# Kernel tuning notes

Measured on AMD Instinct MI355X. Metric: run time of the kernel, lower is better.

Reference implementation:

```python
import jax, jax.numpy as jnp
import numpy as np

# Model dims derived from layers=[1024,2048,2048,2048,2048]
B = 4096
SUM_EVEN = 4096  # 0 + 2048 + 2048
SUM_ODD = 4096   # 2048 + 2048
D1 = 2048        # layers[1]: width of Ux
BLK = 2048


def rho(x):
    return jax.nn.sigmoid(4.0 * (x - 0.5))


def make_mask():
    # Staircase block pattern from layer_slices():
    # (rows 0:2048, cols 0:2048), (rows 0:2048, cols 2048:4096), (rows 2048:4096, cols 2048:4096)
    m = np.zeros((SUM_EVEN, SUM_ODD), dtype=np.float32)
    m[0:BLK, 0:BLK] = 1.0
    m[0:BLK, BLK:2 * BLK] = 1.0
    m[BLK:2 * BLK, BLK:2 * BLK] = 1.0
    return jnp.asarray(m)


def setup_inputs() -> dict:
    key = jax.random.key(0)
    k1, k2, k3 = jax.random.split(key, 3)
    xavier_std = 0.02  # ~ sqrt(2/(2048+2048)) per block
    W_mask = make_mask()
    W_tensor = jax.random.normal(k1, (SUM_EVEN, SUM_ODD), jnp.float32) * xavier_std
    W_tensor = W_tensor * W_mask  # enforce staircase sparsity at init
    return {
        "Ux": jax.random.normal(k2, (B, D1), jnp.float32),
        "s": jax.random.normal(k3, (B, SUM_EVEN), jnp.float32),
        "W_tensor": W_tensor,
        "b_even": jnp.zeros((1, SUM_EVEN), jnp.float32),
        "b_odd": jnp.zeros((1, SUM_ODD), jnp.float32),
        "W_mask": W_mask,
    }


def reference(Ux, s, W_tensor, b_even, b_odd, W_mask):
    # s_new = rho(rho(s) @ W + b_odd [+ Ux on first D1 cols]) @ W.T + b_even
    W = W_tensor * W_mask  # masked staircase matrix
    s_odd = rho(s) @ W + b_odd                 # [B, SUM_ODD]
    s_odd = s_odd.at[:, :D1].add(Ux)           # x only feeds first hidden layer
    return rho(s_odd) @ W.T + b_even           # [B, SUM_EVEN]
```

## Files before the change

### kernel.cpp

```cpp
#include <hip/hip_runtime.h>
#include <hip/hip_bf16.h>


#define N_DIM 4096
#define D1_DIM 2048

typedef short short8 __attribute__((ext_vector_type(8)));
typedef float f32x4 __attribute__((ext_vector_type(4)));

__device__ __forceinline__ float rho_f(float x) {
    return 1.0f / (1.0f + __expf(2.0f - 4.0f * x));
}

__device__ __forceinline__ unsigned short f2bf(float x) {
    unsigned int u = __builtin_bit_cast(unsigned int, x);
    u += 0x7fffu + ((u >> 16) & 1u);
    return (unsigned short)(u >> 16);
}

__device__ __forceinline__ void gl_lds16(const unsigned short* g, void* l) {
    __builtin_amdgcn_global_load_lds(
        (const __attribute__((address_space(1))) void*)g,
        (__attribute__((address_space(3))) void*)l, 16, 0, 0);
}

__global__ __launch_bounds__(256) void prep_kernel(
    const float* __restrict__ s, const float* __restrict__ W,
    unsigned short* __restrict__ Rs, unsigned short* __restrict__ Wb,
    unsigned short* __restrict__ WTb) {
    __shared__ unsigned short t[32][33];
    const int id = blockIdx.x;
    if (id < 16384) {
        const int bx = id & 127, by = id >> 7;
        if (by * 32 >= D1_DIM && bx * 32 < D1_DIM) return;
        const int tx = threadIdx.x & 31, ty = threadIdx.x >> 5;
        const int x = bx * 32 + tx;
        #pragma unroll
        for (int r = 0; r < 4; r++) {
            const int y = by * 32 + ty + r * 8;
            const size_t idx = (size_t)y * N_DIM + x;
            const unsigned short b = f2bf(W[idx]);
            Wb[idx] = b;
            t[ty + r * 8][tx] = b;
        }
        __syncthreads();
        #pragma unroll
        for (int r = 0; r < 4; r++) {
            const int yy = ty + r * 8;
            WTb[(size_t)(bx * 32 + yy) * N_DIM + (by * 32 + tx)] = t[tx][yy];
        }
    } else {
        const int n8 = (N_DIM * N_DIM) / 8;
        const int stride = 2048 * 256;
        for (int i = (id - 16384) * 256 + threadIdx.x; i < n8; i += stride) {
            float4 a = ((const float4*)s)[2 * i];
            float4 b = ((const float4*)s)[2 * i + 1];
            unsigned int r0 = f2bf(rho_f(a.x)) | ((unsigned int)f2bf(rho_f(a.y)) << 16);
            unsigned int r1 = f2bf(rho_f(a.z)) | ((unsigned int)f2bf(rho_f(a.w)) << 16);
            unsigned int r2 = f2bf(rho_f(b.x)) | ((unsigned int)f2bf(rho_f(b.y)) << 16);
            unsigned int r3 = f2bf(rho_f(b.z)) | ((unsigned int)f2bf(rho_f(b.w)) << 16);
            uint4 o; o.x = r0; o.y = r1; o.z = r2; o.w = r3;
            ((uint4*)Rs)[i] = o;
        }
    }
}

template<int MODE>
__global__ __launch_bounds__(1024, 4) void gemm_kernel(
    const unsigned short* __restrict__ A,
    const unsigned short* __restrict__ Bt,
    void* __restrict__ Out,
    const float* __restrict__ Ux,
    const float* __restrict__ bias) {
    __shared__ __align__(16) char lds[163840];

    const int id = blockIdx.x;
    const int wg = ((id & 7) << 5) | (id >> 3);
    const int by = wg >> 4, bx = wg & 15;
    const int brow = by << 8, bcol = bx << 8;

    const int tid = threadIdx.x;
    const int w = tid >> 6;
    const int L = tid & 63;
    const int wr = w >> 2;
    const int wc = w & 3;
    const int fr = L & 15;
    const int fq = L >> 4;
    const int swz = fr & 7;

    int kbeg, kend;
    if (MODE == 1) { kbeg = 0; kend = (bcol < D1_DIM) ? D1_DIM : N_DIM; }
    else           { kbeg = (bcol < D1_DIM) ? 0 : D1_DIM; kend = N_DIM; }

    const int srl = w * 8 + (L >> 3);
    const int schunk8 = ((L & 7) ^ (L >> 3)) << 3;
    const int wbase = w * 1024;
#define STAGEF(mat, gb, kcol, base) do {                                       \
        const unsigned short* g0_ = (mat) +                                    \
            (size_t)((gb) + srl) * N_DIM + (kcol) + schunk8;                   \
        gl_lds16(g0_, lds + (base) + wbase);                                   \
        gl_lds16(g0_ + 128 * N_DIM, lds + (base) + 16384 + wbase);             \
    } while (0)

    short8 af[2][4], bf[4];
#define LDA_K(ab, ks) do {                                                     \
        _Pragma("unroll") for (int m_ = 0; m_ < 4; ++m_) {                     \
            const int R_ = wr * 64 + m_ * 16 + fr;                             \
            af[ks][m_] = *(const short8*)(lds + (ab) + R_ * 128 +              \
                ((((ks) * 4 + fq) ^ swz) << 4)); }                             \
    } while (0)
#define LDB_K(bb, ks) do {                                                     \
        _Pragma("unroll") for (int n_ = 0; n_ < 4; ++n_) {                     \
            const int R_ = wc * 64 + n_ * 16 + fr;                             \
            bf[n_] = *(const short8*)(lds + (bb) + R_ * 128 +                  \
                ((((ks) * 4 + fq) ^ swz) << 4)); }                             \
    } while (0)

    f32x4 acc[4][4];
    #pragma unroll
    for (int i = 0; i < 4; i++)
        #pragma unroll
        for (int j = 0; j < 4; j++)
            acc[i][j] = (f32x4){0.f, 0.f, 0.f, 0.f};

#define MFMA_K(ks) do {                                                        \
        __builtin_amdgcn_s_setprio(1);                                         \
        _Pragma("unroll") for (int m_ = 0; m_ < 4; ++m_)                       \
        _Pragma("unroll") for (int n_ = 0; n_ < 4; ++n_)                       \
            acc[m_][n_] = __builtin_amdgcn_mfma_f32_16x16x32_bf16(             \
                af[ks][m_], bf[n_], acc[m_][n_], 0, 0, 0);                     \
        __builtin_amdgcn_s_setprio(0);                                         \
    } while (0)

#define SBAR0() __builtin_amdgcn_sched_barrier(0)
#define LGKM(n) do { asm volatile("s_waitcnt lgkmcnt(" #n ")" ::: "memory");   \
                     SBAR0(); } while (0)
#define BAR() __builtin_amdgcn_s_barrier()

    const int nk = (kend - kbeg) >> 6;
    const int km = nk - 1;

    {
        const int k0 = kbeg;
        const int k1 = kbeg + ((1 & km) << 6);
        STAGEF(A, brow, k0, 0);       STAGEF(Bt, bcol, k0, 98304);
        STAGEF(A, brow, k1, 32768);   STAGEF(Bt, bcol, k1, 131072);
        asm volatile("s_waitcnt vmcnt(4)" ::: "memory");
        BAR();
    }

    int ai = 0, si = 2;
    for (int t = 0; t < nk; ++t) {
        const int aB = ai * 32768;
        const int sA = si * 32768;
        const int bB = 98304 + (t & 1) * 32768;
        const int ka = kbeg + (((t + 2) & km) << 6);

        STAGEF(A, brow, ka, sA);
        LDA_K(aB, 0); SBAR0();
        LDB_K(bB, 0); SBAR0();
        LDA_K(aB, 1); SBAR0();
        LGKM(4);
        MFMA_K(0);
        LDB_K(bB, 1); SBAR0();
        LGKM(0);
        MFMA_K(1);
        BAR();
        STAGEF(Bt, bcol, ka, bB);
        asm volatile("s_waitcnt vmcnt(4)" ::: "memory");
        BAR();
        ai++; if (ai == 3) ai = 0;
        si++; if (si == 3) si = 0;
    }
    asm volatile("s_waitcnt vmcnt(0)" ::: "memory");

    const bool hasUx = (MODE == 1) && (bcol < D1_DIM);
    #pragma unroll
    for (int m = 0; m < 4; m++) {
        const int row0 = brow + wr * 64 + m * 16 + fq * 4;
        #pragma unroll
        for (int n = 0; n < 4; n++) {
            const int col = bcol + wc * 64 + n * 16 + fr;
            const float bv = bias[col];
            #pragma unroll
            for (int r = 0; r < 4; r++) {
                const int row = row0 + r;
                float v = acc[m][n][r] + bv;
                if (MODE == 1) {
                    if (hasUx) v += Ux[(size_t)row * D1_DIM + col];
                    ((unsigned short*)Out)[(size_t)row * N_DIM + col] =
                        f2bf(rho_f(v));
                } else {
                    ((float*)Out)[(size_t)row * N_DIM + col] = v;
                }
            }
        }
    }
#undef STAGEF
#undef LDA_K
#undef LDB_K
#undef MFMA_K
#undef SBAR0
#undef LGKM
#undef BAR
}

extern "C" void kernel_launch(void* const* d_in, const int* in_sizes, int n_in,
                              void* d_out, int out_size, void* d_ws, size_t ws_size,
                              hipStream_t stream) {
    const float* Ux     = (const float*)d_in[0];
    const float* s      = (const float*)d_in[1];
    const float* W      = (const float*)d_in[2];
    const float* b_even = (const float*)d_in[3];
    const float* b_odd  = (const float*)d_in[4];

    char* ws = (char*)d_ws;
    const size_t SZ = (size_t)N_DIM * N_DIM * 2;
    unsigned short* Rs  = (unsigned short*)(ws);
    unsigned short* R2  = (unsigned short*)(ws + SZ);
    unsigned short* Wb  = (unsigned short*)(ws + 2 * SZ);
    unsigned short* WTb = (unsigned short*)(ws + 3 * SZ);

    prep_kernel<<<18432, 256, 0, stream>>>(s, W, Rs, Wb, WTb);
    gemm_kernel<1><<<256, 1024, 0, stream>>>(Rs, WTb, (void*)R2, Ux, b_odd);
    gemm_kernel<2><<<256, 1024, 0, stream>>>(R2, Wb, d_out, Ux, b_even);
}
```

Before: 248.5 us.

## Shrink GEMM tiles to 256x128 with BK=32 and schedule heavy tiles first

Each GEMM block now covers a 256x128 output tile with 8 waves instead of 256x256 with 16 waves, and the K step drops from 64 to 32. The pipeline is simplified to one three-buffer ring holding A and B, with one barrier per step, using 72KB of LDS instead of 160KB. Blocks are ordered so that the tiles with the longer K range (4096 vs 2048, given the staircase mask) launch first. The aim is better load balance across CUs and more resident blocks, at the cost of less data reuse per tile, more loop iterations and barriers, and removal of the earlier split-fragment MFMA/LDS interleaving.

```diff
diff --git a/kernel.cpp b/kernel.cpp
--- a/kernel.cpp
+++ b/kernel.cpp
@@ -66,110 +66,97 @@
 }
 
 template<int MODE>
-__global__ __launch_bounds__(1024, 4) void gemm_kernel(
+__global__ __launch_bounds__(512, 4) void gemm_kernel(
     const unsigned short* __restrict__ A,
     const unsigned short* __restrict__ Bt,
     void* __restrict__ Out,
     const float* __restrict__ Ux,
     const float* __restrict__ bias) {
-    __shared__ __align__(16) char lds[163840];
+    __shared__ __align__(16) char lds[73728];
 
     const int id = blockIdx.x;
-    const int wg = ((id & 7) << 5) | (id >> 3);
-    const int by = wg >> 4, bx = wg & 15;
-    const int brow = by << 8, bcol = bx << 8;
+    const int grp = id >> 8;
+    const int i = id & 255;
+    const int tile = ((i & 7) << 5) | (i >> 3);
+    const int by = tile >> 4;
+    const int bxg = tile & 15;
+    int bx;
+    if (MODE == 1) bx = grp ? bxg : 16 + bxg;
+    else           bx = grp ? 16 + bxg : bxg;
+    const int brow = by << 8;
+    const int bcol = bx << 7;
 
     const int tid = threadIdx.x;
     const int w = tid >> 6;
     const int L = tid & 63;
-    const int wr = w >> 2;
-    const int wc = w & 3;
+    const int wr = w >> 1;
+    const int wc = w & 1;
     const int fr = L & 15;
     const int fq = L >> 4;
-    const int swz = fr & 7;
 
     int kbeg, kend;
     if (MODE == 1) { kbeg = 0; kend = (bcol < D1_DIM) ? D1_DIM : N_DIM; }
     else           { kbeg = (bcol < D1_DIM) ? 0 : D1_DIM; kend = N_DIM; }
 
-    const int srl = w * 8 + (L >> 3);
-    const int schunk8 = ((L & 7) ^ (L >> 3)) << 3;
-    const int wbase = w * 1024;
-#define STAGEF(mat, gb, kcol, base) do {                                       \
-        const unsigned short* g0_ = (mat) +                                    \
-            (size_t)((gb) + srl) * N_DIM + (kcol) + schunk8;                   \
-        gl_lds16(g0_, lds + (base) + wbase);                                   \
-        gl_lds16(g0_ + 128 * N_DIM, lds + (base) + 16384 + wbase);             \
+    const int srow = tid >> 2;
+    const int schunk = (tid & 3) ^ ((srow >> 1) & 3);
+    const unsigned short* gA0 = A + (size_t)(brow + srow) * N_DIM + schunk * 8;
+    const unsigned short* gA1 = gA0 + 128 * N_DIM;
+    const unsigned short* gB0 = Bt + (size_t)(bcol + srow) * N_DIM + schunk * 8;
+    const int dst16 = tid * 16;
+#define STAGE(kcol, bi) do {                                                   \
+        gl_lds16(gA0 + (kcol), lds + (bi) * 16384 + dst16);                    \
+        gl_lds16(gA1 + (kcol), lds + (bi) * 16384 + 8192 + dst16);             \
+        gl_lds16(gB0 + (kcol), lds + 49152 + (bi) * 8192 + dst16);             \
     } while (0)
 
-    short8 af[2][4], bf[4];
-#define LDA_K(ab, ks) do {                                                     \
-        _Pragma("unroll") for (int m_ = 0; m_ < 4; ++m_) {                     \
-            const int R_ = wr * 64 + m_ * 16 + fr;                             \
-            af[ks][m_] = *(const short8*)(lds + (ab) + R_ * 128 +              \
-                ((((ks) * 4 + fq) ^ swz) << 4)); }                             \
-    } while (0)
-#define LDB_K(bb, ks) do {                                                     \
-        _Pragma("unroll") for (int n_ = 0; n_ < 4; ++n_) {                     \
-            const int R_ = wc * 64 + n_ * 16 + fr;                             \
-            bf[n_] = *(const short8*)(lds + (bb) + R_ * 128 +                  \
-                ((((ks) * 4 + fq) ^ swz) << 4)); }                             \
+    const int slotb = (fq ^ ((fr >> 1) & 3)) << 4;
+    short8 af[4], bf[4];
+#define LDFRAGS(bi) do {                                                       \
+        const char* ab_ = lds + (bi) * 16384;                                  \
+        const char* bb_ = lds + 49152 + (bi) * 8192;                           \
+        _Pragma("unroll") for (int m_ = 0; m_ < 4; ++m_)                       \
+            af[m_] = *(const short8*)(ab_ + (wr * 64 + m_ * 16 + fr) * 64 +    \
+                                      slotb);                                  \
+        _Pragma("unroll") for (int n_ = 0; n_ < 4; ++n_)                       \
+            bf[n_] = *(const short8*)(bb_ + (wc * 64 + n_ * 16 + fr) * 64 +    \
+                                      slotb);                                  \
     } while (0)
 
     f32x4 acc[4][4];
     #pragma unroll
-    for (int i = 0; i < 4; i++)
-        #pragma unroll
-        for (int j = 0; j < 4; j++)
-            acc[i][j] = (f32x4){0.f, 0.f, 0.f, 0.f};
-
-#define MFMA_K(ks) do {                                                        \
-        __builtin_amdgcn_s_setprio(1);                                         \
-        _Pragma("unroll") for (int m_ = 0; m_ < 4; ++m_)                       \
-        _Pragma("unroll") for (int n_ = 0; n_ < 4; ++n_)                       \
-            acc[m_][n_] = __builtin_amdgcn_mfma_f32_16x16x32_bf16(             \
-                af[ks][m_], bf[n_], acc[m_][n_], 0, 0, 0);                     \
-        __builtin_amdgcn_s_setprio(0);                                         \
-    } while (0)
+    for (int m = 0; m < 4; m++)
+        #pragma unroll
+        for (int n = 0; n < 4; n++)
+            acc[m][n] = (f32x4){0.f, 0.f, 0.f, 0.f};
 
 #define SBAR0() __builtin_amdgcn_sched_barrier(0)
-#define LGKM(n) do { asm volatile("s_waitcnt lgkmcnt(" #n ")" ::: "memory");   \
-                     SBAR0(); } while (0)
 #define BAR() __builtin_amdgcn_s_barrier()
 
-    const int nk = (kend - kbeg) >> 6;
+    const int nk = (kend - kbeg) >> 5;
     const int km = nk - 1;
 
-    {
-        const int k0 = kbeg;
-        const int k1 = kbeg + ((1 & km) << 6);
-        STAGEF(A, brow, k0, 0);       STAGEF(Bt, bcol, k0, 98304);
-        STAGEF(A, brow, k1, 32768);   STAGEF(Bt, bcol, k1, 131072);
-        asm volatile("s_waitcnt vmcnt(4)" ::: "memory");
+    STAGE(kbeg, 0);
+    STAGE(kbeg + ((1 & km) << 5), 1);
+    asm volatile("s_waitcnt vmcnt(3)" ::: "memory");
+    BAR();
+
+    int ci = 0, si = 2;
+    for (int t = 0; t < nk; ++t) {
+        const int ka = kbeg + (((t + 2) & km) << 5);
+        STAGE(ka, si);
+        LDFRAGS(ci);
+        asm volatile("s_waitcnt lgkmcnt(0)" ::: "memory");
+        SBAR0();
+        #pragma unroll
+        for (int m = 0; m < 4; ++m)
+            #pragma unroll
+            for (int n = 0; n < 4; ++n)
+                acc[m][n] = __builtin_amdgcn_mfma_f32_16x16x32_bf16(
+                    af[m], bf[n], acc[m][n], 0, 0, 0);
+        asm volatile("s_waitcnt vmcnt(3)" ::: "memory");
         BAR();
-    }
-
-    int ai = 0, si = 2;
-    for (int t = 0; t < nk; ++t) {
-        const int aB = ai * 32768;
-        const int sA = si * 32768;
-        const int bB = 98304 + (t & 1) * 32768;
-        const int ka = kbeg + (((t + 2) & km) << 6);
-
-        STAGEF(A, brow, ka, sA);
-        LDA_K(aB, 0); SBAR0();
-        LDB_K(bB, 0); SBAR0();
-        LDA_K(aB, 1); SBAR0();
-        LGKM(4);
-        MFMA_K(0);
-        LDB_K(bB, 1); SBAR0();
-        LGKM(0);
-        MFMA_K(1);
-        BAR();
-        STAGEF(Bt, bcol, ka, bB);
-        asm volatile("s_waitcnt vmcnt(4)" ::: "memory");
-        BAR();
-        ai++; if (ai == 3) ai = 0;
+        ci++; if (ci == 3) ci = 0;
         si++; if (si == 3) si = 0;
     }
     asm volatile("s_waitcnt vmcnt(0)" ::: "memory");
@@ -196,12 +183,9 @@
             }
         }
     }
-#undef STAGEF
-#undef LDA_K
-#undef LDB_K
-#undef MFMA_K
+#undef STAGE
+#undef LDFRAGS
 #undef SBAR0
-#undef LGKM
 #undef BAR
 }
 
@@ -222,6 +206,6 @@
     unsigned short* WTb = (unsigned short*)(ws + 3 * SZ);
 
     prep_kernel<<<18432, 256, 0, stream>>>(s, W, Rs, Wb, WTb);
-    gemm_kernel<1><<<256, 1024, 0, stream>>>(Rs, WTb, (void*)R2, Ux, b_odd);
-    gemm_kernel<2><<<256, 1024, 0, stream>>>(R2, Wb, d_out, Ux, b_even);
-}
+    gemm_kernel<1><<<512, 512, 0, stream>>>(Rs, WTb, (void*)R2, Ux, b_odd);
+    gemm_kernel<2><<<512, 512, 0, stream>>>(R2, Wb, d_out, Ux, b_even);
+}
```

Result: slower. 272.2 us (+9.6%).
